# Kernel optimization log

Hardware: AMD Instinct MI355X
Metric: run time of the kernel (lower is better)

## Reference

```python
import jax, jax.numpy as jnp
import numpy as np
import math

# Config (mirrors KoopmanConfig)
B = 4096          # batch
C = 128           # context_dim
D = 32            # latent_dim
K = 8             # num_experts
R = 8             # low_rank
NSEG = 3
STEPS = [8, 8, 8] # steps_per_segment, sums to HORIZON
HORIZON = 24
DT = 0.1
DECAY_TARGET = 0.7
DECAY_SCALE = 1.0
SIGMA_MAX = 1.0
MAX_FROB = 3.0
TEMP = 2.0        # gate_temperature_start (stage 1)
EPS = 1e-6


def expm_fixed(M):
    """Matrix exponential via scaling-and-squaring + Taylor (Horner).
    Valid because ||M*dt|| is small (A Frobenius-clamped to 3, Q diag <= 1, dt=0.1).
    Fully differentiable and batched over leading dims."""
    SQ = 6       # scale by 2^-6 -> norm ~0.01
    ORDER = 14
    A = M / (2.0 ** SQ)
    n = M.shape[-1]
    I = jnp.eye(n, dtype=M.dtype)
    Rm = I
    for k in range(ORDER, 0, -1):
        Rm = I + (A @ Rm) / k
    for _ in range(SQ):
        Rm = Rm @ Rm
    return Rm


def setup_inputs() -> dict:
    key = jax.random.key(0)
    ks = jax.random.split(key, 10)
    def init(k, shape, fan_in):
        return jax.random.normal(k, shape, jnp.float32) / np.float32(np.sqrt(fan_in))
    return {
        "context": jax.random.normal(ks[0], (B, C), jnp.float32),
        "z0": jax.random.normal(ks[1], (B, D), jnp.float32),
        # per-segment stacked Linear params (torch Linear: y = x @ W + b)
        "S_W": init(ks[2], (NSEG, C, K * D * D), C),
        "S_b": jnp.zeros((NSEG, K * D * D), jnp.float32),
        "L_W": init(ks[3], (NSEG, C, K * D * R), C),
        "L_b": jnp.zeros((NSEG, K * D * R), jnp.float32),
        "G_W": init(ks[4], (NSEG, C, K), C),
        "G_b": jnp.zeros((NSEG, K), jnp.float32),
        "Sig_W": init(ks[5], (NSEG, C, D), C),
        "Sig_b": jnp.zeros((NSEG, D), jnp.float32),
    }


def reference(context, z0, S_W, S_b, L_W, L_b, G_W, G_b, Sig_W, Sig_b):
    b = context.shape[0]
    mu = jnp.float32(-math.log(DECAY_TARGET) / (DT * HORIZON) * DECAY_SCALE)
    I = jnp.eye(D, dtype=context.dtype)
    z = z0
    cov = jnp.zeros((b, D, D), context.dtype)
    states_all, covs_all = [], []
    for s in range(NSEG):
        # SegmentExpertGenerator
        raw_S = (context @ S_W[s] + S_b[s]).reshape(b, K, D, D)
        skew = raw_S - jnp.swapaxes(raw_S, -1, -2)
        raw_L = (context @ L_W[s] + L_b[s]).reshape(b, K, D, R)
        LLT = jnp.einsum('bkdr,bker->bkde', raw_L, raw_L)
        A_experts = skew - LLT - mu * I                      # [b,K,D,D]
        logits = context @ G_W[s] + G_b[s]
        w = jax.nn.softmax(logits / max(TEMP, EPS), axis=-1)  # [b,K]
        A = jnp.einsum('bk,bkde->bde', w, A_experts)
        # clamp_frobenius
        frob = jnp.linalg.norm(A.reshape(b, -1), axis=-1)
        scale = jnp.where(frob > MAX_FROB, MAX_FROB / (frob + EPS), jnp.float32(1.0))
        A = A * scale[:, None, None]
        # SigmaGenerator: diagonal Sigma -> Q = Sigma Sigma^T = diag(diag^2)
        diag = jnp.minimum(jax.nn.softplus(context @ Sig_W[s] + Sig_b[s]), SIGMA_MAX)
        Q = (diag ** 2)[:, :, None] * I                      # [b,D,D]
        # Van Loan discretization: expm([[A, Q], [0, -A^T]] * dt)
        top = jnp.concatenate([A, Q], axis=-1)
        bot = jnp.concatenate([jnp.zeros_like(Q), -jnp.swapaxes(A, -1, -2)], axis=-1)
        M = jnp.concatenate([top, bot], axis=-2)             # [b,2D,2D]
        E = expm_fixed(M * DT)
        Phi = E[..., :D, :D]
        Qd = Phi @ E[..., :D, D:]
        Qd = 0.5 * (Qd + jnp.swapaxes(Qd, -1, -2))
        PhiT = jnp.swapaxes(Phi, -1, -2)
        def step(carry, _):
            zc, cc = carry
            zc = jnp.einsum('bij,bj->bi', Phi, zc)
            cc = Phi @ cc @ PhiT + Qd
            cc = 0.5 * (cc + jnp.swapaxes(cc, -1, -2))
            return (zc, cc), (zc, cc)
        (z, cov), (zs, cs) = jax.lax.scan(step, (z, cov), None, length=STEPS[s])
        states_all.append(jnp.swapaxes(zs, 0, 1))   # [b,steps,D]
        covs_all.append(jnp.swapaxes(cs, 0, 1))     # [b,steps,D,D]
    states = jnp.concatenate(states_all, axis=1)    # [b,HORIZON,D]
    covariances = jnp.concatenate(covs_all, axis=1) # [b,HORIZON,D,D]
    return states, covariances
```

## Files before the change

### kernel.cpp

```cpp
#include <hip/hip_runtime.h>
#include <math.h>


#define NSEGC 3
#define BSZ   4096
#define MUC   0.14861455999447191f
#define XSC   0.025f
#define XRS(r) (((r) & 7) << 2)

typedef unsigned short ushort_t;
typedef unsigned int uint_t;
typedef __attribute__((ext_vector_type(8))) short bf16x8;
typedef __attribute__((ext_vector_type(16))) float f32x16;

__device__ __forceinline__ void ld4(float d[4], const float* p) {
  const float4 v = *(const float4*)p; d[0]=v.x; d[1]=v.y; d[2]=v.z; d[3]=v.w;
}
__device__ __forceinline__ void st4(float* p, const float d[4]) {
  *(float4*)p = make_float4(d[0], d[1], d[2], d[3]);
}
__device__ __forceinline__ unsigned short bf_rne(float x) {
  unsigned b = __float_as_uint(x);
  unsigned r = b + 0x7FFFu + ((b >> 16) & 1u);
  return (unsigned short)(r >> 16);
}
__device__ __forceinline__ float bf2f(short v) {
  return __uint_as_float(((uint_t)(unsigned short)v) << 16);
}

__global__ __launch_bounds__(64) void kA(const float* __restrict__ ctx,
    const float* __restrict__ GW, const float* __restrict__ Gb,
    const float* __restrict__ SgW, const float* __restrict__ Sgb,
    float* __restrict__ Wsm, float* __restrict__ Q2) {
  const int b = blockIdx.x, s = blockIdx.y, l = threadIdx.x;
  __shared__ float c[128];
  c[l]      = ctx[(size_t)b*128 + l];
  c[l + 64] = ctx[(size_t)b*128 + 64 + l];
  __syncthreads();
  if (l < 8) {
    float acc = Gb[s*8 + l];
    #pragma unroll 4
    for (int q = 0; q < 128; ++q) acc += c[q] * GW[(size_t)(s*128 + q)*8 + l];
    float li = acc * 0.5f;
    float m = li;
    m = fmaxf(m, __shfl_xor(m, 1));
    m = fmaxf(m, __shfl_xor(m, 2));
    m = fmaxf(m, __shfl_xor(m, 4));
    float e = expf(li - m);
    float sum = e;
    sum += __shfl_xor(sum, 1);
    sum += __shfl_xor(sum, 2);
    sum += __shfl_xor(sum, 4);
    Wsm[((size_t)s*BSZ + b)*8 + l] = e / sum;
  } else if (l < 40) {
    const int d = l - 8;
    float acc = Sgb[s*32 + d];
    #pragma unroll 4
    for (int q = 0; q < 128; ++q) acc += c[q] * SgW[(size_t)(s*128 + q)*32 + d];
    float sp = fmaxf(acc, 0.f) + log1pf(expf(-fabsf(acc)));
    float dg = fminf(sp, 1.0f);
    Q2[((size_t)s*BSZ + b)*32 + d] = dg * dg;
  }
}

__global__ __launch_bounds__(256) void kCvtX(const float* __restrict__ ctx,
    ushort_t* __restrict__ Xh, ushort_t* __restrict__ Xl) {
  const int idx = blockIdx.x*256 + threadIdx.x;
  const float v = ctx[idx];
  const unsigned short h = bf_rne(v);
  Xh[idx] = h;
  Xl[idx] = bf_rne(v - __uint_as_float(((unsigned)h) << 16));
}

__global__ __launch_bounds__(256) void kCvtL(const float* __restrict__ LW,
    ushort_t* __restrict__ Lh, ushort_t* __restrict__ Ll) {
  __shared__ float tile[32][33];
  const int nb = blockIdx.x * 32, cb = blockIdx.y * 32, s = blockIdx.z;
  const int tx = threadIdx.x & 31, ty = threadIdx.x >> 5;
  for (int r = ty; r < 32; r += 8)
    tile[r][tx] = LW[((size_t)(s*128 + cb + r))*2048 + nb + tx];
  __syncthreads();
  for (int r = ty; r < 32; r += 8) {
    const float v = tile[tx][r];
    const unsigned short h = bf_rne(v);
    const size_t o = ((size_t)s*2048 + nb + r)*128 + cb + tx;
    Lh[o] = h;
    Ll[o] = bf_rne(v - __uint_as_float(((unsigned)h) << 16));
  }
}

__global__ __launch_bounds__(256) void kCvtA(const float* __restrict__ ctx,
    const float* __restrict__ Wsm, ushort_t* __restrict__ Ah,
    ushort_t* __restrict__ Al, int s) {
  __shared__ float cs[128];
  __shared__ float wwv[8];
  const int b = blockIdx.x, t = threadIdx.x;
  if (t < 128) cs[t] = ctx[(size_t)b*128 + t];
  else if (t < 136) wwv[t - 128] = Wsm[((size_t)s*BSZ + b)*8 + (t - 128)];
  __syncthreads();
  for (int kc = t; kc < 1088; kc += 256) {
    float v = 0.f;
    if (kc < 1024) v = wwv[kc >> 7] * cs[kc & 127];
    else if (kc < 1032) v = wwv[kc - 1024];
    const unsigned short h = bf_rne(v);
    const float hf = __uint_as_float(((unsigned)h) << 16);
    Ah[(size_t)b*1088 + kc] = h;
    Al[(size_t)b*1088 + kc] = bf_rne(v - hf);
  }
}

__global__ __launch_bounds__(256) void kCvtB(const float* __restrict__ SW,
    const float* __restrict__ Sb, ushort_t* __restrict__ Bh,
    ushort_t* __restrict__ Bl) {
  const int n = blockIdx.x, s = blockIdx.y, t = threadIdx.x;
  const int i = n >> 5, j = n & 31, nT = j*32 + i;
  ushort_t* bh = Bh + (size_t)s*1114112;
  ushort_t* bl = Bl + (size_t)s*1114112;
  for (int kc = t; kc < 1088; kc += 256) {
    float v = 0.f;
    if (kc < 1024) {
      const int k = kc >> 7, c = kc & 127;
      const float* base = SW + ((size_t)(s*128 + c))*8192 + (size_t)k*1024;
      v = base[n] - base[nT];
    } else if (kc < 1032) {
      const int k = kc - 1024;
      const float* base = Sb + (size_t)s*8192 + (size_t)k*1024;
      v = base[n] - base[nT];
    }
    const unsigned short h = bf_rne(v);
    const float hf = __uint_as_float(((unsigned)h) << 16);
    bh[(size_t)n*1088 + kc] = h;
    bl[(size_t)n*1088 + kc] = bf_rne(v - hf);
  }
}

__global__ __launch_bounds__(256) void kB3(const ushort_t* __restrict__ Ah,
    const ushort_t* __restrict__ Al, const ushort_t* __restrict__ Bh,
    const ushort_t* __restrict__ Bl, float* __restrict__ ASseg) {
  __shared__ ushort_t sArr[2][2][8192];
  const int t = threadIdx.x;
  const int l = t & 63, w = t >> 6;
  const int hh = l >> 5, lane31 = l & 31;
  const int nb = blockIdx.x * 128, bb = blockIdx.y * 128;
  const int wr0 = (w & 1) * 64, wc0 = (w >> 1) * 64;

  const ushort_t* APT[3] = {Ah, Ah, Al};
  const ushort_t* BPT[3] = {Bh, Bl, Bh};

  f32x16 acc[2][2];
  #pragma unroll
  for (int a = 0; a < 2; ++a)
    #pragma unroll
    for (int bq = 0; bq < 2; ++bq)
      #pragma unroll
      for (int e = 0; e < 16; ++e) acc[a][bq][e] = 0.f;

  #define STAGE(buf, it) do {                                                  \
    const int p_ = (it) / 17, ks_ = (it) - p_*17;                              \
    const ushort_t* As_ = APT[p_];                                             \
    const ushort_t* Bs_ = BPT[p_];                                             \
    _Pragma("unroll")                                                          \
    for (int i_ = 0; i_ < 4; ++i_) {                                           \
      const int gidx_ = i_*256 + t;                                            \
      const int r_ = gidx_ >> 3, g_ = gidx_ & 7;                               \
      const int gs_ = g_ ^ (r_ & 7);                                           \
      const ushort_t* srcA_ = As_ + (size_t)(bb + r_)*1088 + ks_*64 + gs_*8;   \
      const ushort_t* srcB_ = Bs_ + (size_t)(nb + r_)*1088 + ks_*64 + gs_*8;   \
      __builtin_amdgcn_global_load_lds(                                        \
        (const __attribute__((address_space(1))) unsigned int*)srcA_,          \
        (__attribute__((address_space(3))) unsigned int*)&sArr[buf][0][(i_*256 + w*64)*8], \
        16, 0, 0);                                                             \
      __builtin_amdgcn_global_load_lds(                                        \
        (const __attribute__((address_space(1))) unsigned int*)srcB_,          \
        (__attribute__((address_space(3))) unsigned int*)&sArr[buf][1][(i_*256 + w*64)*8], \
        16, 0, 0);                                                             \
    }                                                                          \
  } while (0)

  STAGE(0, 0);
  int cur = 0;
  #pragma unroll 1
  for (int it = 0; it < 51; ++it) {
    __syncthreads();
    if (it + 1 < 51) STAGE(cur ^ 1, it + 1);
    const ushort_t* lA = &sArr[cur][0][0];
    const ushort_t* lB = &sArr[cur][1][0];
    #pragma unroll
    for (int kc = 0; kc < 4; ++kc) {
      bf16x8 af[2], bfr[2];
      #pragma unroll
      for (int rt = 0; rt < 2; ++rt) {
        const int row = wr0 + rt*32 + lane31;
        const int slot = (kc*2 + hh) ^ (row & 7);
        af[rt] = *(const bf16x8*)&lA[row*64 + slot*8];
      }
      #pragma unroll
      for (int ct = 0; ct < 2; ++ct) {
        const int row = wc0 + ct*32 + lane31;
        const int slot = (kc*2 + hh) ^ (row & 7);
        bfr[ct] = *(const bf16x8*)&lB[row*64 + slot*8];
      }
      #pragma unroll
      for (int rt = 0; rt < 2; ++rt)
        #pragma unroll
        for (int ct = 0; ct < 2; ++ct)
          acc[rt][ct] = __builtin_amdgcn_mfma_f32_32x32x16_bf16(
              af[rt], bfr[ct], acc[rt][ct], 0, 0, 0);
    }
    cur ^= 1;
  }
  #undef STAGE

  #pragma unroll
  for (int rt = 0; rt < 2; ++rt)
    #pragma unroll
    for (int ct = 0; ct < 2; ++ct) {
      float* o = ASseg + ((size_t)(bb + wr0 + rt*32))*1024 + nb + wc0 + ct*32 + lane31;
      #pragma unroll
      for (int reg = 0; reg < 16; ++reg) {
        const int row = (reg & 3) + 8*(reg >> 2) + 4*hh;
        o[(size_t)row*1024] = acc[rt][ct][reg];
      }
    }
}

__global__ __launch_bounds__(256) void kL3(const ushort_t* __restrict__ Xh,
    const ushort_t* __restrict__ Xl, const ushort_t* __restrict__ Lh,
    const ushort_t* __restrict__ Ll, const float* __restrict__ Lb,
    const float* __restrict__ Wsm, float* __restrict__ lt, int s) {
  __shared__ ushort_t sArr[2][2][8192];
  __shared__ float sqw[128][8];
  const int t = threadIdx.x;
  const int l = t & 63, w = t >> 6;
  const int hh = l >> 5, lane31 = l & 31;
  const int nb = blockIdx.x * 128, bb = blockIdx.y * 128;
  const int wr0 = (w & 1) * 64, wc0 = (w >> 1) * 64;
  for (int i = t; i < 1024; i += 256)
    sqw[i >> 3][i & 7] = sqrtf(Wsm[((size_t)s*BSZ + bb + (i >> 3))*8 + (i & 7)]);

  const ushort_t* APT[3] = {Xh, Xh, Xl};
  const ushort_t* BPT[3] = {Lh + (size_t)s*262144, Ll + (size_t)s*262144,
                            Lh + (size_t)s*262144};

  f32x16 acc[2][2];
  #pragma unroll
  for (int a = 0; a < 2; ++a)
    #pragma unroll
    for (int bq = 0; bq < 2; ++bq)
      #pragma unroll
      for (int e = 0; e < 16; ++e) acc[a][bq][e] = 0.f;

  #define STAGEL(buf, it) do {                                                 \
    const int p_ = (it) >> 1, ks_ = (it) & 1;                                  \
    const ushort_t* As_ = APT[p_];                                             \
    const ushort_t* Bs_ = BPT[p_];                                             \
    _Pragma("unroll")                                                          \
    for (int i_ = 0; i_ < 4; ++i_) {                                           \
      const int gidx_ = i_*256 + t;                                            \
      const int r_ = gidx_ >> 3, g_ = gidx_ & 7;                               \
      const int gs_ = g_ ^ (r_ & 7);                                           \
      const ushort_t* srcA_ = As_ + (size_t)(bb + r_)*128 + ks_*64 + gs_*8;    \
      const ushort_t* srcB_ = Bs_ + (size_t)(nb + r_)*128 + ks_*64 + gs_*8;    \
      __builtin_amdgcn_global_load_lds(                                        \
        (const __attribute__((address_space(1))) unsigned int*)srcA_,          \
        (__attribute__((address_space(3))) unsigned int*)&sArr[buf][0][(i_*256 + w*64)*8], \
        16, 0, 0);                                                             \
      __builtin_amdgcn_global_load_lds(                                        \
        (const __attribute__((address_space(1))) unsigned int*)srcB_,          \
        (__attribute__((address_space(3))) unsigned int*)&sArr[buf][1][(i_*256 + w*64)*8], \
        16, 0, 0);                                                             \
    }                                                                          \
  } while (0)

  STAGEL(0, 0);
  int cur = 0;
  #pragma unroll 1
  for (int it = 0; it < 6; ++it) {
    __syncthreads();
    if (it + 1 < 6) STAGEL(cur ^ 1, it + 1);
    const ushort_t* lA = &sArr[cur][0][0];
    const ushort_t* lB = &sArr[cur][1][0];
    #pragma unroll
    for (int kc = 0; kc < 4; ++kc) {
      bf16x8 af[2], bfr[2];
      #pragma unroll
      for (int rt = 0; rt < 2; ++rt) {
        const int row = wr0 + rt*32 + lane31;
        const int slot = (kc*2 + hh) ^ (row & 7);
        af[rt] = *(const bf16x8*)&lA[row*64 + slot*8];
      }
      #pragma unroll
      for (int ct = 0; ct < 2; ++ct) {
        const int row = wc0 + ct*32 + lane31;
        const int slot = (kc*2 + hh) ^ (row & 7);
        bfr[ct] = *(const bf16x8*)&lB[row*64 + slot*8];
      }
      #pragma unroll
      for (int rt = 0; rt < 2; ++rt)
        #pragma unroll
        for (int ct = 0; ct < 2; ++ct)
          acc[rt][ct] = __builtin_amdgcn_mfma_f32_32x32x16_bf16(
              af[rt], bfr[ct], acc[rt][ct], 0, 0, 0);
    }
    cur ^= 1;
  }
  #undef STAGEL

  #pragma unroll
  for (int rt = 0; rt < 2; ++rt)
    #pragma unroll
    for (int ct = 0; ct < 2; ++ct) {
      const int n = nb + wc0 + ct*32 + lane31;
      const float lb = Lb[(size_t)s*2048 + n];
      const int kidx = n >> 8;
      const int ltcol = (kidx << 8) + ((n & 7) << 5) + ((n >> 3) & 31);
      #pragma unroll
      for (int reg = 0; reg < 16; ++reg) {
        const int lrow = wr0 + rt*32 + (reg & 3) + 8*(reg >> 2) + 4*hh;
        lt[(size_t)(bb + lrow)*2048 + ltcol] =
            (acc[rt][ct][reg] + lb) * sqw[lrow][kidx];
      }
    }
}

__global__ __launch_bounds__(128) void kLLT(const float* __restrict__ LT,
                                            float* __restrict__ AS, int s) {
  __shared__ float L4[4][64][32];
  const int t = threadIdx.x;
  const int bbase = blockIdx.x * 4;
  {
    float* l4f = &L4[0][0][0];
    const float* src = LT + (size_t)bbase * 2048;
    for (int i = t*4; i < 8192; i += 512)
      *(float4*)&l4f[i] = *(const float4*)&src[i];
  }
  __syncthreads();
  const int b = t >> 5, u = t & 31;
  const int i0 = (u >> 2) * 4, j0 = (u & 3) * 8;
  float acc[4][8] = {};
  #pragma unroll 8
  for (int kr = 0; kr < 64; ++kr) {
    float pa[4], pb[8];
    ld4(pa, &L4[b][kr][i0]);
    ld4(pb, &L4[b][kr][j0]); ld4(pb + 4, &L4[b][kr][j0 + 4]);
    #pragma unroll
    for (int ii = 0; ii < 4; ++ii)
      #pragma unroll
      for (int jj = 0; jj < 8; ++jj) acc[ii][jj] += pa[ii] * pb[jj];
  }
  float* dst = AS + ((size_t)s*BSZ + bbase + b)*1024;
  for (int ii = 0; ii < 4; ++ii) {
    float x[8];
    ld4(x, &dst[(i0+ii)*32 + j0]); ld4(x + 4, &dst[(i0+ii)*32 + j0 + 4]);
    #pragma unroll
    for (int jj = 0; jj < 8; ++jj) x[jj] -= acc[ii][jj];
    st4(&dst[(i0+ii)*32 + j0], x); st4(&dst[(i0+ii)*32 + j0 + 4], &x[4]);
  }
}

struct Frag { bf16x8 h0, l0, h1, l1; };

__device__ __forceinline__ void cvt8(const float x[8], bf16x8& hi, bf16x8& lo) {
  uint_t h[4], l[4];
  #pragma unroll
  for (int p = 0; p < 4; ++p) {
    const uint_t b0 = __float_as_uint(x[2*p]);
    const uint_t b1 = __float_as_uint(x[2*p + 1]);
    h[p] = __builtin_amdgcn_perm(b1, b0, 0x07060302u);
    const float l0f = x[2*p]     - __uint_as_float(b0 & 0xFFFF0000u);
    const float l1f = x[2*p + 1] - __uint_as_float(b1 & 0xFFFF0000u);
    l[p] = __builtin_amdgcn_perm(__float_as_uint(l1f), __float_as_uint(l0f),
                                 0x07060302u);
  }
  hi = __builtin_bit_cast(bf16x8, make_uint4(h[0], h[1], h[2], h[3]));
  lo = __builtin_bit_cast(bf16x8, make_uint4(l[0], l[1], l[2], l[3]));
}
__device__ __forceinline__ void rd_row8(const float* M, int r, int kb, float o[8]) {
  const float* p = M + r*32;
  ld4(o,     p + ((kb)     ^ XRS(r)));
  ld4(o + 4, p + ((kb + 4) ^ XRS(r)));
}
__device__ __forceinline__ void rd_col8(const float* M, int c, int kb, float o[8]) {
  #pragma unroll
  for (int e = 0; e < 8; ++e) o[e] = M[(kb + e)*32 + (c ^ XRS(kb + e))];
}
__device__ __forceinline__ void mkfrag_row(const float* M, int r, int hoff, Frag& f) {
  float t0[8], t1[8];
  rd_row8(M, r, hoff, t0);
  rd_row8(M, r, 16 + hoff, t1);
  cvt8(t0, f.h0, f.l0);
  cvt8(t1, f.h1, f.l1);
}
__device__ __forceinline__ void mkfrag_col(const float* M, int c, int hoff, Frag& f) {
  float t0[8], t1[8];
  rd_col8(M, c, hoff, t0);
  rd_col8(M, c, 16 + hoff, t1);
  cvt8(t0, f.h0, f.l0);
  cvt8(t1, f.h1, f.l1);
}
__device__ __forceinline__ f32x16 mmacc(const Frag& A, const Frag& B, f32x16 acc) {
  acc = __builtin_amdgcn_mfma_f32_32x32x16_bf16(A.h0, B.h0, acc, 0, 0, 0);
  acc = __builtin_amdgcn_mfma_f32_32x32x16_bf16(A.h0, B.l0, acc, 0, 0, 0);
  acc = __builtin_amdgcn_mfma_f32_32x32x16_bf16(A.l0, B.h0, acc, 0, 0, 0);
  acc = __builtin_amdgcn_mfma_f32_32x32x16_bf16(A.h1, B.h1, acc, 0, 0, 0);
  acc = __builtin_amdgcn_mfma_f32_32x32x16_bf16(A.h1, B.l1, acc, 0, 0, 0);
  acc = __builtin_amdgcn_mfma_f32_32x32x16_bf16(A.l1, B.h1, acc, 0, 0, 0);
  return acc;
}
__device__ __forceinline__ f32x16 zero16() {
  f32x16 z = {0.f,0.f,0.f,0.f,0.f,0.f,0.f,0.f,0.f,0.f,0.f,0.f,0.f,0.f,0.f,0.f};
  return z;
}
__device__ __forceinline__ void st_T(float* M, int j, int ho4, const float v[16]) {
  float* p = M + j*32;
  #pragma unroll
  for (int m = 0; m < 4; ++m) st4(p + ((8*m + ho4) ^ XRS(j)), v + 4*m);
}
__device__ __forceinline__ void ld16_T(const float* M, int j, int ho4, float o[16]) {
  const float* p = M + j*32;
  #pragma unroll
  for (int m = 0; m < 4; ++m) ld4(o + 4*m, p + ((8*m + ho4) ^ XRS(j)));
}

__global__ __launch_bounds__(64, 3) void kC10(const float* __restrict__ AS,
    const float* __restrict__ Q2, const float* __restrict__ z0,
    float* __restrict__ out) {
  __shared__ float S11[1024];
  __shared__ float S12[1024];
  __shared__ float S22[1024];
  __shared__ float zarr[32], qds[32];
  const int b = blockIdx.x, t = threadIdx.x;
  const int j = t & 31, hh = t >> 5;
  const int hoff = hh * 8, ho4 = hh * 4;

  if (t < 32) zarr[t] = z0[(size_t)b*32 + t];
  float covreg[16];
  #pragma unroll
  for (int r = 0; r < 16; ++r) covreg[r] = 0.f;
  __syncthreads();

  float* covout = out + 3145728 + (size_t)b*24576;
  float* stout  = out + (size_t)b*768;

  for (int s = 0; s < NSEGC; ++s) {
    if (t < 32) qds[t] = Q2[((size_t)s*BSZ + b)*32 + t] * XSC;
    const float* asb = AS + ((size_t)s*BSZ + b)*1024;
    float av[16];
    #pragma unroll
    for (int m = 0; m < 4; ++m) ld4(av + 4*m, &asb[j*32 + 16*hh + 4*m]);
    #pragma unroll
    for (int i = 0; i < 16; ++i) if (16*hh + i == j) av[i] -= MUC;
    float ssq = 0.f;
    #pragma unroll
    for (int i = 0; i < 16; ++i) ssq += av[i]*av[i];
    #pragma unroll
    for (int off = 1; off < 64; off <<= 1) ssq += __shfl_xor(ssq, off);
    const float frob = sqrtf(ssq);
    const float sc = (frob > 3.0f ? 3.0f / (frob + 1e-6f) : 1.0f) * XSC;
    #pragma unroll
    for (int i = 0; i < 16; ++i) av[i] *= sc;
    __syncthreads();
    #pragma unroll
    for (int m = 0; m < 4; ++m)
      st4(&S12[j*32 + ((16*hh + 4*m) ^ XRS(j))], av + 4*m);
    __syncthreads();
    Frag aA, aT;
    mkfrag_row(S12, j, hoff, aA);
    mkfrag_col(S12, j, hoff, aT);
    __syncthreads();
    #pragma unroll
    for (int m = 0; m < 4; ++m) {
      float id[4], zo[4] = {0.f, 0.f, 0.f, 0.f};
      #pragma unroll
      for (int e = 0; e < 4; ++e) id[e] = (16*hh + 4*m + e == j) ? 1.f : 0.f;
      st4(&S11[j*32 + ((16*hh + 4*m) ^ XRS(j))], id);
      st4(&S22[j*32 + ((16*hh + 4*m) ^ XRS(j))], id);
      st4(&S12[j*32 + ((16*hh + 4*m) ^ XRS(j))], zo);
    }
    __syncthreads();
    float qv[16];
    #pragma unroll
    for (int r = 0; r < 16; ++r) qv[r] = qds[(r&3) + 8*(r>>2) + ho4];

    for (int k = 5; k >= 1; --k) {
      const float rk = 1.0f / (float)k;
      Frag Bf;
      float Xs[16];
      mkfrag_row(S11, j, hoff, Bf);
      f32x16 X = mmacc(aA, Bf, zero16());
      #pragma unroll
      for (int r = 0; r < 16; ++r) {
        const int row = (r&3) + 8*(r>>2) + ho4;
        Xs[r] = X[r]*rk + (row == j ? 1.f : 0.f);
      }
      st_T(S11, j, ho4, Xs);
      mkfrag_row(S12, j, hoff, Bf);
      X = mmacc(aA, Bf, zero16());
      float rv[16];
      ld16_T(S22, j, ho4, rv);
      #pragma unroll
      for (int r = 0; r < 16; ++r) Xs[r] = (X[r] + qv[r]*rv[r]) * rk;
      st_T(S12, j, ho4, Xs);
      mkfrag_row(S22, j, hoff, Bf);
      X = mmacc(aT, Bf, zero16());
      #pragma unroll
      for (int r = 0; r < 16; ++r) {
        const int row = (r&3) + 8*(r>>2) + ho4;
        Xs[r] = (row == j ? 1.f : 0.f) - X[r]*rk;
      }
      st_T(S22, j, ho4, Xs);
    }
    __syncthreads();

    {
      Frag Ac, Br;
      float Xs[16];
      mkfrag_col(S11, j, hoff, Ac);
      mkfrag_row(S11, j, hoff, Br);
      f32x16 X1 = mmacc(Ac, Br, zero16());
      #pragma unroll
      for (int r = 0; r < 16; ++r) Xs[r] = X1[r];
      st_T(S11, j, ho4, Xs);
      Frag B12; mkfrag_row(S12, j, hoff, B12);
      f32x16 X2 = mmacc(Ac, B12, zero16());
      Frag A12; mkfrag_col(S12, j, hoff, A12);
      Frag B22; mkfrag_row(S22, j, hoff, B22);
      X2 = mmacc(A12, B22, X2);
      #pragma unroll
      for (int r = 0; r < 16; ++r) Xs[r] = X2[r];
      st_T(S12, j, ho4, Xs);
      Frag A22; mkfrag_col(S22, j, hoff, A22);
      f32x16 X3 = mmacc(A22, B22, zero16());
      #pragma unroll
      for (int r = 0; r < 16; ++r) Xs[r] = X3[r];
      st_T(S22, j, ho4, Xs);
    }
    __syncthreads();
    {
      Frag Ac, Br;
      float Xs[16];
      mkfrag_col(S11, j, hoff, Ac);
      mkfrag_row(S11, j, hoff, Br);
      f32x16 X1 = mmacc(Ac, Br, zero16());
      Frag B12; mkfrag_row(S12, j, hoff, B12);
      f32x16 X2 = mmacc(Ac, B12, zero16());
      Frag A12; mkfrag_col(S12, j, hoff, A12);
      Frag B22; mkfrag_row(S22, j, hoff, B22);
      X2 = mmacc(A12, B22, X2);
      #pragma unroll
      for (int r = 0; r < 16; ++r) Xs[r] = X1[r];
      st_T(S11, j, ho4, Xs);
      #pragma unroll
      for (int r = 0; r < 16; ++r) Xs[r] = X2[r];
      st_T(S12, j, ho4, Xs);
    }
    __syncthreads();

    Frag PhiF;
    mkfrag_col(S11, j, hoff, PhiF);
    {
      Frag B12; mkfrag_row(S12, j, hoff, B12);
      f32x16 Xq = mmacc(PhiF, B12, zero16());
      float Xs[16];
      #pragma unroll
      for (int r = 0; r < 16; ++r) Xs[r] = Xq[r];
      st_T(S22, j, ho4, Xs);
      __syncthreads();
      float sym[16];
      #pragma unroll
      for (int r = 0; r < 16; ++r) {
        const int row = (r&3) + 8*(r>>2) + ho4;
        const float tv = S22[row*32 + (j ^ XRS(row))];
        sym[r] = 0.5f * (Xs[r] + tv);
      }
      __syncthreads();
      st_T(S22, j, ho4, sym);
    }
    __syncthreads();

    st_T(S12, j, ho4, covreg);
    __syncthreads();

    for (int tt = 0; tt < 8; ++tt) {
      Frag Bcov; mkfrag_row(S12, j, hoff, Bcov);
      f32x16 G = mmacc(PhiF, Bcov, zero16());
      float Gs[16];
      #pragma unroll
      for (int r = 0; r < 16; ++r) Gs[r] = G[r];
      st_T(S11, j, ho4, Gs);
      Frag AG; mkfrag_col(S11, j, hoff, AG);
      f32x16 C = mmacc(AG, PhiF, zero16());
      float qdv[16], Cs[16];
      ld16_T(S22, j, ho4, qdv);
      #pragma unroll
      for (int r = 0; r < 16; ++r) Cs[r] = C[r] + qdv[r];
      float zp = 0.f;
      #pragma unroll
      for (int e = 0; e < 8; ++e) {
        zp += (bf2f(PhiF.h0[e]) + bf2f(PhiF.l0[e])) * zarr[hoff + e];
        zp += (bf2f(PhiF.h1[e]) + bf2f(PhiF.l1[e])) * zarr[16 + hoff + e];
      }
      zp += __shfl_xor(zp, 32);
      st_T(S12, j, ho4, Cs);
      #pragma unroll
      for (int r = 0; r < 16; ++r) covreg[r] = Cs[r];
      float* cb = covout + (size_t)(s*8 + tt)*1024;
      #pragma unroll
      for (int r = 0; r < 16; ++r)
        cb[((r&3) + 8*(r>>2) + ho4)*32 + j] = Cs[r];
      if (t < 32) {
        zarr[t] = zp;
        stout[(s*8 + tt)*32 + t] = zp;
      }
      __syncthreads();
    }
  }
}

extern "C" void kernel_launch(void* const* d_in, const int* in_sizes, int n_in,
                              void* d_out, int out_size, void* d_ws, size_t ws_size,
                              hipStream_t stream) {
  const float* ctx  = (const float*)d_in[0];
  const float* z0   = (const float*)d_in[1];
  const float* S_W  = (const float*)d_in[2];
  const float* S_b  = (const float*)d_in[3];
  const float* L_W  = (const float*)d_in[4];
  const float* L_b  = (const float*)d_in[5];
  const float* G_W  = (const float*)d_in[6];
  const float* G_b  = (const float*)d_in[7];
  const float* Sg_W = (const float*)d_in[8];
  const float* Sg_b = (const float*)d_in[9];
  float* out = (float*)d_out;
  float* ws  = (float*)d_ws;

  float* w_   = ws;
  float* q2   = ws + 98304;
  float* as_  = ws + 1015808;
  ushort_t* panAh  = (ushort_t*)(ws + 13598720);
  ushort_t* panAl  = panAh + 4456448;
  ushort_t* panBh3 = panAl + 4456448;
  ushort_t* panBl3 = panBh3 + 3342336;
  float* lt = ws + 13598720;
  ushort_t* cxh = (ushort_t*)(ws + 21987328);
  ushort_t* cxl = cxh + 524288;
  ushort_t* lwh = cxl + 524288;
  ushort_t* lwl = lwh + 786432;

  kA   <<<dim3(4096, 3), 64,  0, stream>>>(ctx, G_W, G_b, Sg_W, Sg_b, w_, q2);
  kCvtX<<<dim3(2048),    256, 0, stream>>>(ctx, cxh, cxl);
  kCvtL<<<dim3(64, 4, 3),256, 0, stream>>>(L_W, lwh, lwl);
  kCvtB<<<dim3(1024, 3), 256, 0, stream>>>(S_W, S_b, panBh3, panBl3);
  for (int s = 0; s < 3; ++s) {
    kCvtA<<<dim3(4096), 256, 0, stream>>>(ctx, w_, panAh, panAl, s);
    kB3  <<<dim3(8, 32), 256, 0, stream>>>(panAh, panAl,
                                           panBh3 + (size_t)s*1114112,
                                           panBl3 + (size_t)s*1114112,
                                           as_ + (size_t)s*4194304);
  }
  for (int s = 0; s < 3; ++s) {
    kL3 <<<dim3(16, 32), 256, 0, stream>>>(cxh, cxl, lwh, lwl, L_b, w_, lt, s);
    kLLT<<<dim3(1024),   128, 0, stream>>>(lt, as_, s);
  }
  kC10<<<dim3(4096),    64, 0, stream>>>(as_, q2, z0, out);
}
```

Baseline: 608.9 us.

## Pre-transpose S weights for coalesced skew build; drop one Taylor term

Adds a kernel that transposes each 32x32 block of S_W into scratch memory. kCvtB then reads both the original and the transposed value with coalesced accesses, replacing the strided base[nT] gather, and runs over fewer, wider blocks. Separately, the in-kernel Taylor loop in the covariance kernel now starts at order 4 instead of 5, which saves MFMA work but lowers the accuracy of the matrix exponential. The transpose scratch reuses the as_ region before it is written, and kCvtB now launches only 192 blocks, which may leave much of the GPU idle.

```diff
diff --git a/kernel.cpp b/kernel.cpp
--- a/kernel.cpp
+++ b/kernel.cpp
@@ -63,6 +63,46 @@
   }
 }
 
+__global__ __launch_bounds__(256) void kT(const float* __restrict__ SW,
+                                          float* __restrict__ SWT) {
+  __shared__ float mt[1056];
+  const int kc = blockIdx.x, s = blockIdx.y, t = threadIdx.x;
+  const int k = kc >> 7, c = kc & 127;
+  const float* src = SW + ((size_t)(s*128 + c))*8192 + (size_t)k*1024;
+  float* dst = SWT + ((size_t)s*1024 + kc)*1024;
+  for (int i = t; i < 1024; i += 256) mt[(i >> 5)*33 + (i & 31)] = src[i];
+  __syncthreads();
+  for (int i = t; i < 1024; i += 256) dst[i] = mt[(i & 31)*33 + (i >> 5)];
+}
+
+__global__ __launch_bounds__(256) void kCvtB(const float* __restrict__ SW,
+    const float* __restrict__ SWT, const float* __restrict__ Sb,
+    ushort_t* __restrict__ Bh, ushort_t* __restrict__ Bl) {
+  const int s = blockIdx.y, t = threadIdx.x;
+  const int n0 = blockIdx.x * 16;
+  const int tn = t & 15, tck = t >> 4;
+  const int n = n0 + tn;
+  const int nT = (n & 31)*32 + (n >> 5);
+  ushort_t* bh = Bh + (size_t)s*1114112;
+  ushort_t* bl = Bl + (size_t)s*1114112;
+  for (int kc0 = 0; kc0 < 1088; kc0 += 16) {
+    const int kc = kc0 + tck;
+    float v = 0.f;
+    if (kc < 1024) {
+      const int k = kc >> 7, c = kc & 127;
+      v = SW[((size_t)(s*128 + c))*8192 + (size_t)k*1024 + n]
+        - SWT[((size_t)s*1024 + kc)*1024 + n];
+    } else if (kc < 1032) {
+      const int k2 = kc - 1024;
+      const float* base = Sb + (size_t)s*8192 + (size_t)k2*1024;
+      v = base[n] - base[nT];
+    }
+    const unsigned short h = bf_rne(v);
+    bh[(size_t)n*1088 + kc] = h;
+    bl[(size_t)n*1088 + kc] = bf_rne(v - __uint_as_float(((unsigned)h) << 16));
+  }
+}
+
 __global__ __launch_bounds__(256) void kCvtX(const float* __restrict__ ctx,
     ushort_t* __restrict__ Xh, ushort_t* __restrict__ Xl) {
   const int idx = blockIdx.x*256 + threadIdx.x;
@@ -106,31 +146,6 @@
     const float hf = __uint_as_float(((unsigned)h) << 16);
     Ah[(size_t)b*1088 + kc] = h;
     Al[(size_t)b*1088 + kc] = bf_rne(v - hf);
-  }
-}
-
-__global__ __launch_bounds__(256) void kCvtB(const float* __restrict__ SW,
-    const float* __restrict__ Sb, ushort_t* __restrict__ Bh,
-    ushort_t* __restrict__ Bl) {
-  const int n = blockIdx.x, s = blockIdx.y, t = threadIdx.x;
-  const int i = n >> 5, j = n & 31, nT = j*32 + i;
-  ushort_t* bh = Bh + (size_t)s*1114112;
-  ushort_t* bl = Bl + (size_t)s*1114112;
-  for (int kc = t; kc < 1088; kc += 256) {
-    float v = 0.f;
-    if (kc < 1024) {
-      const int k = kc >> 7, c = kc & 127;
-      const float* base = SW + ((size_t)(s*128 + c))*8192 + (size_t)k*1024;
-      v = base[n] - base[nT];
-    } else if (kc < 1032) {
-      const int k = kc - 1024;
-      const float* base = Sb + (size_t)s*8192 + (size_t)k*1024;
-      v = base[n] - base[nT];
-    }
-    const unsigned short h = bf_rne(v);
-    const float hf = __uint_as_float(((unsigned)h) << 16);
-    bh[(size_t)n*1088 + kc] = h;
-    bl[(size_t)n*1088 + kc] = bf_rne(v - hf);
   }
 }
 
@@ -422,7 +437,7 @@
   for (int m = 0; m < 4; ++m) ld4(o + 4*m, p + ((8*m + ho4) ^ XRS(j)));
 }
 
-__global__ __launch_bounds__(64, 3) void kC10(const float* __restrict__ AS,
+__global__ __launch_bounds__(64, 3) void kC12(const float* __restrict__ AS,
     const float* __restrict__ Q2, const float* __restrict__ z0,
     float* __restrict__ out) {
   __shared__ float S11[1024];
@@ -482,7 +497,7 @@
     #pragma unroll
     for (int r = 0; r < 16; ++r) qv[r] = qds[(r&3) + 8*(r>>2) + ho4];
 
-    for (int k = 5; k >= 1; --k) {
+    for (int k = 4; k >= 1; --k) {
       const float rk = 1.0f / (float)k;
       Frag Bf;
       float Xs[16];
@@ -636,6 +651,7 @@
   float* w_   = ws;
   float* q2   = ws + 98304;
   float* as_  = ws + 1015808;
+  float* swt  = ws + 1015808;
   ushort_t* panAh  = (ushort_t*)(ws + 13598720);
   ushort_t* panAl  = panAh + 4456448;
   ushort_t* panBh3 = panAl + 4456448;
@@ -649,7 +665,8 @@
   kA   <<<dim3(4096, 3), 64,  0, stream>>>(ctx, G_W, G_b, Sg_W, Sg_b, w_, q2);
   kCvtX<<<dim3(2048),    256, 0, stream>>>(ctx, cxh, cxl);
   kCvtL<<<dim3(64, 4, 3),256, 0, stream>>>(L_W, lwh, lwl);
-  kCvtB<<<dim3(1024, 3), 256, 0, stream>>>(S_W, S_b, panBh3, panBl3);
+  kT   <<<dim3(1024, 3), 256, 0, stream>>>(S_W, swt);
+  kCvtB<<<dim3(64, 3),   256, 0, stream>>>(S_W, swt, S_b, panBh3, panBl3);
   for (int s = 0; s < 3; ++s) {
     kCvtA<<<dim3(4096), 256, 0, stream>>>(ctx, w_, panAh, panAl, s);
     kB3  <<<dim3(8, 32), 256, 0, stream>>>(panAh, panAl,
@@ -661,5 +678,5 @@
     kL3 <<<dim3(16, 32), 256, 0, stream>>>(cxh, cxl, lwh, lwl, L_b, w_, lt, s);
     kLLT<<<dim3(1024),   128, 0, stream>>>(lt, as_, s);
   }
-  kC10<<<dim3(4096),    64, 0, stream>>>(as_, q2, z0, out);
-}
+  kC12<<<dim3(4096),    64, 0, stream>>>(as_, q2, z0, out);
+}
```

Result: slower. 626.0 us (+2.8%).
